# Kernel tuning notes

Measured on AMD Instinct MI355X. Metric: run time of the kernel, lower is better.

The kernel has to match this reference:

```python
import jax, jax.numpy as jnp
import numpy as np

DIM = 8
EPS = 1e-6
TRIL = DIM * (DIM + 1) // 2  # 36


def _build_L(params):
    # params: [N, TRIL] -> lower-triangular L: [N, DIM, DIM] with diag clamped >= 1e-4
    rows, cols = jnp.tril_indices(DIM)
    L = jnp.zeros((params.shape[0], DIM, DIM), params.dtype)
    L = L.at[:, rows, cols].set(params)
    idx = jnp.arange(DIM)
    d = jnp.clip(L[:, idx, idx], 0.0001)
    return L.at[:, idx, idx].set(d)


def _compute_density(L):
    # L: [N, DIM, DIM] -> PSD trace-1 density matrices [N, DIM, DIM]
    I = jnp.eye(DIM, dtype=L.dtype)
    rho = jnp.einsum('nij,nkj->nik', L, L) + EPS * I
    w = jnp.linalg.eigvalsh(rho)                      # [N, DIM]
    corr = jnp.maximum(-w.min(axis=-1), 0.0) + 1e-6   # shift to PSD
    rho = rho + corr[:, None, None] * I
    tr = jnp.trace(rho, axis1=1, axis2=2)
    return rho / (tr[:, None, None] + EPS)


def _matrix_sqrt(x):
    U, S, Vh = jnp.linalg.svd(x, full_matrices=False)
    sqrt_S = jnp.sqrt(S + EPS)
    return (U * sqrt_S[..., None, :]) @ Vh


def _quantum_fidelity(rho, sigma):
    sqrt_rho = _matrix_sqrt(rho)
    product = sqrt_rho @ sigma @ sqrt_rho
    S = jnp.linalg.svd(product, compute_uv=False)
    f = jnp.sum(jnp.sqrt(S + EPS), axis=-1)
    return jnp.clip(f, 0.0, 1.0)


def setup_inputs() -> dict:
    key = jax.random.key(0)
    k1, k2, k3 = jax.random.split(key, 3)
    B, S, V = 16384, 10, 100000
    contexts = jax.random.randint(k1, (B, S), 0, V)
    targets = jax.random.randint(k2, (B,), 0, V)
    # embedding table, init roughly like the torch module (uniform + diag ramp)
    emb_weight = jax.random.uniform(k3, (V, TRIL), jnp.float32, -0.1, 0.1)
    diag_idx = np.array([i * (i + 1) // 2 + i for i in range(DIM)])
    diag_vals = jnp.linspace(0.1, 1.0, DIM, dtype=jnp.float32)
    emb_weight = emb_weight.at[:, diag_idx].set(jnp.broadcast_to(diag_vals, (V, DIM)))
    return {"contexts": contexts, "targets": targets, "emb_weight": emb_weight}


def reference(contexts, targets, emb_weight):
    B, S = contexts.shape
    # context density matrices
    ctx_params = jnp.take(emb_weight, contexts.reshape(-1), axis=0)   # [B*S, TRIL]
    rho_ctx = _compute_density(_build_L(ctx_params)).reshape(B, S, DIM, DIM)
    mask = (contexts != 0).astype(rho_ctx.dtype)[:, :, None, None]
    context_rho = (rho_ctx * mask).sum(axis=1) / mask.sum(axis=1)     # [B, DIM, DIM]
    # target density matrices
    tgt_params = jnp.take(emb_weight, targets, axis=0)                # [B, TRIL]
    rho_tgt = _compute_density(_build_L(tgt_params))                  # [B, DIM, DIM]
    f = _quantum_fidelity(context_rho, rho_tgt)                       # [B]
    return -jnp.log(jnp.clip(f, 1e-8))
```

## Files before the change

kernel.cpp:

```cpp
#include <hip/hip_runtime.h>
#include <math.h>

#define NB   16384
#define SEQ  10
#define DIM  8
#define TRIL 36

__device__ __forceinline__ constexpr int tri(int r, int c) { return r * (r + 1) / 2 + c; }

__device__ __forceinline__ double fast_rsqrt(double x) {
    double r = __builtin_amdgcn_rsq(x);
    r = r * (1.5 - 0.5 * x * r * r);
    r = r * (1.5 - 0.5 * x * r * r);
    return r;
}
__device__ __forceinline__ double fast_rcp(double x) {
    double r = __builtin_amdgcn_rcp(x);
    r = r * (2.0 - x * r);
    r = r * (2.0 - x * r);
    return r;
}
__device__ __forceinline__ double fast_sqrt(double x) { return x * fast_rsqrt(x); }

template <bool ACCUM>
__device__ __forceinline__ void add_density(const float* __restrict__ p, double (&dst)[TRIL]) {
    double L[TRIL];
    #pragma unroll
    for (int i = 0; i < TRIL; ++i) L[i] = (double)p[i];
    #pragma unroll
    for (int d = 0; d < DIM; ++d) L[tri(d, d)] = fmax(L[tri(d, d)], 1.0e-4);

    double tr = 1.6e-5;
    #pragma unroll
    for (int i = 0; i < TRIL; ++i) tr += L[i] * L[i];
    double inv = fast_rcp(tr + 1.0e-6);

    #pragma unroll
    for (int i = 0; i < DIM; ++i) {
        #pragma unroll
        for (int j = 0; j <= i; ++j) {
            double sum = (i == j) ? 2.0e-6 : 0.0;
            #pragma unroll
            for (int k = 0; k <= j; ++k) sum += L[tri(i, k)] * L[tri(j, k)];
            if (ACCUM) dst[tri(i, j)] += sum * inv;
            else       dst[tri(i, j)]  = sum * inv;
        }
    }
}

__global__ void __launch_bounds__(64)
qcbow_kernel(const int* __restrict__ contexts,
             const int* __restrict__ targets,
             const float* __restrict__ emb,
             float* __restrict__ out)
{
    int b = blockIdx.x * 64 + threadIdx.x;

    double A[TRIL];
    #pragma unroll
    for (int i = 0; i < TRIL; ++i) A[i] = 0.0;
    double cnt = 0.0;

    for (int s = 0; s < SEQ; ++s) {
        int tok = contexts[b * SEQ + s];
        if (tok != 0) {
            add_density<true>(emb + (size_t)tok * TRIL, A);
            cnt += 1.0;
        }
    }
    double invc = fast_rcp(cnt);
    #pragma unroll
    for (int i = 0; i < TRIL; ++i) A[i] *= invc;
    #pragma unroll
    for (int d = 0; d < DIM; ++d) A[tri(d, d)] += 1.0e-6;

    double sig[TRIL];
    add_density<false>(emb + (size_t)targets[b] * TRIL, sig);

    #pragma unroll
    for (int j = 0; j < DIM; ++j) {
        double d = A[tri(j, j)];
        #pragma unroll
        for (int k = 0; k < j; ++k) d -= A[tri(j, k)] * A[tri(j, k)];
        d = fmax(d, 1.0e-30);
        double invd = fast_rsqrt(d);
        A[tri(j, j)] = d * invd;
        #pragma unroll
        for (int i = j + 1; i < DIM; ++i) {
            double v = A[tri(i, j)];
            #pragma unroll
            for (int k = 0; k < j; ++k) v -= A[tri(i, k)] * A[tri(j, k)];
            A[tri(i, j)] = v * invd;
        }
    }

    double C[TRIL];
    #pragma unroll
    for (int j = 0; j < DIM; ++j) {
        double w[DIM];
        #pragma unroll
        for (int k = 0; k < DIM; ++k) {
            double sum = 0.0;
            #pragma unroll
            for (int l = j; l < DIM; ++l) {
                double sk = (k >= l) ? sig[tri(k, l)] : sig[tri(l, k)];
                sum += sk * A[tri(l, j)];
            }
            w[k] = sum;
        }
        #pragma unroll
        for (int i = 0; i <= j; ++i) {
            double sum = 0.0;
            #pragma unroll
            for (int k = i; k < DIM; ++k) sum += A[tri(k, i)] * w[k];
            C[tri(j, i)] = sum;
        }
    }

    for (int sweep = 0; sweep < 8; ++sweep) {
        #pragma unroll
        for (int p = 0; p < DIM - 1; ++p) {
            #pragma unroll
            for (int q = p + 1; q < DIM; ++q) {
                double apq = C[tri(q, p)];
                if (fabs(apq) > 1.0e-20) {
                    double app = C[tri(p, p)];
                    double aqq = C[tri(q, q)];
                    float tauf = ((float)aqq - (float)app) * (0.5f * __builtin_amdgcn_rcpf((float)apq));
                    float tf = __builtin_amdgcn_rcpf(fabsf(tauf) + sqrtf(1.0f + tauf * tauf));
                    tf = (tauf >= 0.0f) ? tf : -tf;
                    double t = (double)tf;
                    double x = 1.0 + t * t;
                    double c = (double)__builtin_amdgcn_rsqf((float)x);
                    c = c * (1.5 - 0.5 * x * c * c);
                    double s = t * c;
                    double cc = c * c, ss = s * s, cs = c * s;
                    C[tri(p, p)] = cc * app + ss * aqq - 2.0 * cs * apq;
                    C[tri(q, q)] = ss * app + cc * aqq + 2.0 * cs * apq;
                    C[tri(q, p)] = cs * (app - aqq) + (cc - ss) * apq;
                    #pragma unroll
                    for (int k = 0; k < DIM; ++k) {
                        if (k == p || k == q) continue;
                        const int ikp = (k > p) ? tri(k, p) : tri(p, k);
                        const int ikq = (k > q) ? tri(k, q) : tri(q, k);
                        double akp = C[ikp];
                        double akq = C[ikq];
                        C[ikp] = c * akp - s * akq;
                        C[ikq] = s * akp + c * akq;
                    }
                }
            }
        }
        if (sweep >= 2) {
            double off2 = 0.0;
            #pragma unroll
            for (int i = 1; i < DIM; ++i) {
                #pragma unroll
                for (int j = 0; j < i; ++j) off2 += C[tri(i, j)] * C[tri(i, j)];
            }
            if (__all(off2 < 1.0e-14)) break;
        }
    }

    double f = 0.0;
    #pragma unroll
    for (int d = 0; d < DIM; ++d) f += fast_sqrt(fabs(C[tri(d, d)]) + 1.0e-6);
    f = fmin(f, 1.0);
    f = fmax(f, 1.0e-8);
    out[b] = (float)(-log(f));
}

extern "C" void kernel_launch(void* const* d_in, const int* in_sizes, int n_in,
                              void* d_out, int out_size, void* d_ws, size_t ws_size,
                              hipStream_t stream) {
    const int*   contexts = (const int*)d_in[0];
    const int*   targets  = (const int*)d_in[1];
    const float* emb      = (const float*)d_in[2];
    float*       out      = (float*)d_out;

    qcbow_kernel<<<dim3(NB / 64), dim3(64), 0, stream>>>(contexts, targets, emb, out);
}
```

Before: 99.73 us.

## Split each batch item across four lanes with parallel one-sided Jacobi SVD

Each batch element is now handled by a group of four lanes instead of one thread. The lanes split the context tokens, combine their density sums with xor shuffles, and each Cholesky-factor the target matrix redundantly. Fidelity comes from a one-sided (Hestenes) Jacobi on the columns of L_A^T L_W, two columns per lane, rotated among lanes in a round-robin order, in place of a two-sided Jacobi on a packed symmetric matrix. Embedding rows are now read with float4 vector loads and kept in float registers. This gives four times as many threads and less serial work per thread, at the cost of redundant Cholesky work, shuffle traffic, and float4 loads that assume 16-byte alignment of 36-float rows (144 bytes, so this holds).

```diff
diff --git a/kernel.cpp b/kernel.cpp
--- a/kernel.cpp
+++ b/kernel.cpp
@@ -24,15 +24,19 @@
 
 template <bool ACCUM>
 __device__ __forceinline__ void add_density(const float* __restrict__ p, double (&dst)[TRIL]) {
-    double L[TRIL];
-    #pragma unroll
-    for (int i = 0; i < TRIL; ++i) L[i] = (double)p[i];
-    #pragma unroll
-    for (int d = 0; d < DIM; ++d) L[tri(d, d)] = fmax(L[tri(d, d)], 1.0e-4);
+    float Lf[TRIL];
+    const float4* p4 = (const float4*)p;
+    #pragma unroll
+    for (int i = 0; i < 9; ++i) {
+        float4 v = p4[i];
+        Lf[4*i+0] = v.x; Lf[4*i+1] = v.y; Lf[4*i+2] = v.z; Lf[4*i+3] = v.w;
+    }
+    #pragma unroll
+    for (int d = 0; d < DIM; ++d) Lf[tri(d, d)] = fmaxf(Lf[tri(d, d)], 1.0e-4f);
 
     double tr = 1.6e-5;
     #pragma unroll
-    for (int i = 0; i < TRIL; ++i) tr += L[i] * L[i];
+    for (int i = 0; i < TRIL; ++i) { double v = (double)Lf[i]; tr += v * v; }
     double inv = fast_rcp(tr + 1.0e-6);
 
     #pragma unroll
@@ -41,9 +45,28 @@
         for (int j = 0; j <= i; ++j) {
             double sum = (i == j) ? 2.0e-6 : 0.0;
             #pragma unroll
-            for (int k = 0; k <= j; ++k) sum += L[tri(i, k)] * L[tri(j, k)];
+            for (int k = 0; k <= j; ++k) sum += (double)Lf[tri(i, k)] * (double)Lf[tri(j, k)];
             if (ACCUM) dst[tri(i, j)] += sum * inv;
             else       dst[tri(i, j)]  = sum * inv;
+        }
+    }
+}
+
+__device__ __forceinline__ void chol36(double (&M)[TRIL]) {
+    #pragma unroll
+    for (int j = 0; j < DIM; ++j) {
+        double d = M[tri(j, j)];
+        #pragma unroll
+        for (int k = 0; k < j; ++k) d -= M[tri(j, k)] * M[tri(j, k)];
+        d = fmax(d, 1.0e-30);
+        double invd = fast_rsqrt(d);
+        M[tri(j, j)] = d * invd;
+        #pragma unroll
+        for (int i = j + 1; i < DIM; ++i) {
+            double v = M[tri(i, j)];
+            #pragma unroll
+            for (int k = 0; k < j; ++k) v -= M[tri(i, k)] * M[tri(j, k)];
+            M[tri(i, j)] = v * invd;
         }
     }
 }
@@ -54,120 +77,123 @@
              const float* __restrict__ emb,
              float* __restrict__ out)
 {
-    int b = blockIdx.x * 64 + threadIdx.x;
+    const int tid = blockIdx.x * 64 + threadIdx.x;
+    const int b = tid >> 2;
+    const int g = threadIdx.x & 3;
 
     double A[TRIL];
     #pragma unroll
     for (int i = 0; i < TRIL; ++i) A[i] = 0.0;
     double cnt = 0.0;
-
-    for (int s = 0; s < SEQ; ++s) {
+    for (int s = g; s < SEQ; s += 4) {
         int tok = contexts[b * SEQ + s];
         if (tok != 0) {
             add_density<true>(emb + (size_t)tok * TRIL, A);
             cnt += 1.0;
         }
     }
+
+    double W[TRIL];
+    add_density<false>(emb + (size_t)targets[b] * TRIL, W);
+
+    #pragma unroll
+    for (int i = 0; i < TRIL; ++i) A[i] += __shfl_xor(A[i], 1, 4);
+    cnt += __shfl_xor(cnt, 1, 4);
+    #pragma unroll
+    for (int i = 0; i < TRIL; ++i) A[i] += __shfl_xor(A[i], 2, 4);
+    cnt += __shfl_xor(cnt, 2, 4);
+
+    chol36(W);
+
     double invc = fast_rcp(cnt);
     #pragma unroll
     for (int i = 0; i < TRIL; ++i) A[i] *= invc;
     #pragma unroll
     for (int d = 0; d < DIM; ++d) A[tri(d, d)] += 1.0e-6;
-
-    double sig[TRIL];
-    add_density<false>(emb + (size_t)targets[b] * TRIL, sig);
-
-    #pragma unroll
-    for (int j = 0; j < DIM; ++j) {
-        double d = A[tri(j, j)];
-        #pragma unroll
-        for (int k = 0; k < j; ++k) d -= A[tri(j, k)] * A[tri(j, k)];
-        d = fmax(d, 1.0e-30);
-        double invd = fast_rsqrt(d);
-        A[tri(j, j)] = d * invd;
-        #pragma unroll
-        for (int i = j + 1; i < DIM; ++i) {
-            double v = A[tri(i, j)];
-            #pragma unroll
-            for (int k = 0; k < j; ++k) v -= A[tri(i, k)] * A[tri(j, k)];
-            A[tri(i, j)] = v * invd;
-        }
-    }
-
-    double C[TRIL];
-    #pragma unroll
-    for (int j = 0; j < DIM; ++j) {
-        double w[DIM];
-        #pragma unroll
-        for (int k = 0; k < DIM; ++k) {
-            double sum = 0.0;
-            #pragma unroll
-            for (int l = j; l < DIM; ++l) {
-                double sk = (k >= l) ? sig[tri(k, l)] : sig[tri(l, k)];
-                sum += sk * A[tri(l, j)];
+    chol36(A);
+
+    double wa[DIM], wb[DIM];
+#define PICKW(JA, JB)                                                              \
+    {                                                                              \
+        _Pragma("unroll")                                                          \
+        for (int k = 0; k < DIM; ++k) wa[k] = (k >= (JA)) ? W[tri(k, (JA))] : 0.0; \
+        _Pragma("unroll")                                                          \
+        for (int k = 0; k < DIM; ++k) wb[k] = (k >= (JB)) ? W[tri(k, (JB))] : 0.0; \
+    }
+    switch (g) {
+        case 0: PICKW(0, 1); break;
+        case 1: PICKW(2, 3); break;
+        case 2: PICKW(4, 5); break;
+        default: PICKW(6, 7); break;
+    }
+#undef PICKW
+
+    double a[DIM], bc[DIM];
+    #pragma unroll
+    for (int i = 0; i < DIM; ++i) {
+        double sa = 0.0, sb = 0.0;
+        #pragma unroll
+        for (int k = i; k < DIM; ++k) {
+            double lk = A[tri(k, i)];
+            sa += lk * wa[k];
+            sb += lk * wb[k];
+        }
+        a[i] = sa; bc[i] = sb;
+    }
+
+    for (int sweep = 0; sweep < 10; ++sweep) {
+        double maxz2 = 0.0;
+        #pragma unroll
+        for (int r = 0; r < 7; ++r) {
+            double x = 0.0, y = 0.0, z = 0.0;
+            #pragma unroll
+            for (int k = 0; k < DIM; ++k) {
+                x += a[k] * a[k];
+                y += bc[k] * bc[k];
+                z += a[k] * bc[k];
             }
-            w[k] = sum;
-        }
-        #pragma unroll
-        for (int i = 0; i <= j; ++i) {
-            double sum = 0.0;
-            #pragma unroll
-            for (int k = i; k < DIM; ++k) sum += A[tri(k, i)] * w[k];
-            C[tri(j, i)] = sum;
-        }
-    }
-
-    for (int sweep = 0; sweep < 8; ++sweep) {
-        #pragma unroll
-        for (int p = 0; p < DIM - 1; ++p) {
-            #pragma unroll
-            for (int q = p + 1; q < DIM; ++q) {
-                double apq = C[tri(q, p)];
-                if (fabs(apq) > 1.0e-20) {
-                    double app = C[tri(p, p)];
-                    double aqq = C[tri(q, q)];
-                    float tauf = ((float)aqq - (float)app) * (0.5f * __builtin_amdgcn_rcpf((float)apq));
-                    float tf = __builtin_amdgcn_rcpf(fabsf(tauf) + sqrtf(1.0f + tauf * tauf));
-                    tf = (tauf >= 0.0f) ? tf : -tf;
-                    double t = (double)tf;
-                    double x = 1.0 + t * t;
-                    double c = (double)__builtin_amdgcn_rsqf((float)x);
-                    c = c * (1.5 - 0.5 * x * c * c);
-                    double s = t * c;
-                    double cc = c * c, ss = s * s, cs = c * s;
-                    C[tri(p, p)] = cc * app + ss * aqq - 2.0 * cs * apq;
-                    C[tri(q, q)] = ss * app + cc * aqq + 2.0 * cs * apq;
-                    C[tri(q, p)] = cs * (app - aqq) + (cc - ss) * apq;
-                    #pragma unroll
-                    for (int k = 0; k < DIM; ++k) {
-                        if (k == p || k == q) continue;
-                        const int ikp = (k > p) ? tri(k, p) : tri(p, k);
-                        const int ikq = (k > q) ? tri(k, q) : tri(q, k);
-                        double akp = C[ikp];
-                        double akq = C[ikq];
-                        C[ikp] = c * akp - s * akq;
-                        C[ikq] = s * akp + c * akq;
-                    }
+            double z2 = z * z;
+            maxz2 = fmax(maxz2, z2);
+            if (z2 > 1.0e-20) {
+                float tauf = (float)(y - x) * (0.5f * __builtin_amdgcn_rcpf((float)z));
+                float tf = __builtin_amdgcn_rcpf(fabsf(tauf) + sqrtf(1.0f + tauf * tauf));
+                tf = (tauf >= 0.0f) ? tf : -tf;
+                double t = (double)tf;
+                double x2 = 1.0 + t * t;
+                double c = (double)__builtin_amdgcn_rsqf((float)x2);
+                c = c * (1.5 - 0.5 * x2 * c * c);
+                double s = t * c;
+                #pragma unroll
+                for (int k = 0; k < DIM; ++k) {
+                    double na = c * a[k] - s * bc[k];
+                    double nb = s * a[k] + c * bc[k];
+                    a[k] = na; bc[k] = nb;
                 }
             }
-        }
-        if (sweep >= 2) {
-            double off2 = 0.0;
-            #pragma unroll
-            for (int i = 1; i < DIM; ++i) {
-                #pragma unroll
-                for (int j = 0; j < i; ++j) off2 += C[tri(i, j)] * C[tri(i, j)];
+            #pragma unroll
+            for (int k = 0; k < DIM; ++k) {
+                double olda = a[k];
+                double sa = (g == 0) ? bc[k] : a[k];
+                double ta = __shfl(sa, (g + 3) & 3, 4);
+                double tb = __shfl(bc[k], (g + 1) & 3, 4);
+                a[k]  = (g == 0) ? olda : ta;
+                bc[k] = (g == 3) ? olda : tb;
             }
-            if (__all(off2 < 1.0e-14)) break;
-        }
-    }
-
-    double f = 0.0;
-    #pragma unroll
-    for (int d = 0; d < DIM; ++d) f += fast_sqrt(fabs(C[tri(d, d)]) + 1.0e-6);
-    f = fmin(f, 1.0);
-    f = fmax(f, 1.0e-8);
-    out[b] = (float)(-log(f));
+        }
+        if (sweep >= 2 && __all(maxz2 < 1.0e-18)) break;
+    }
+
+    double x = 0.0, y = 0.0;
+    #pragma unroll
+    for (int k = 0; k < DIM; ++k) { x += a[k] * a[k]; y += bc[k] * bc[k]; }
+    double fp = fast_sqrt(x + 1.0e-6) + fast_sqrt(y + 1.0e-6);
+    fp += __shfl_xor(fp, 1, 4);
+    fp += __shfl_xor(fp, 2, 4);
+    if (g == 0) {
+        double f = fmin(fp, 1.0);
+        f = fmax(f, 1.0e-8);
+        out[b] = (float)(-log(f));
+    }
 }
 
 extern "C" void kernel_launch(void* const* d_in, const int* in_sizes, int n_in,
@@ -178,5 +204,5 @@
     const float* emb      = (const float*)d_in[2];
     float*       out      = (float*)d_out;
 
-    qcbow_kernel<<<dim3(NB / 64), dim3(64), 0, stream>>>(contexts, targets, emb, out);
-}
+    qcbow_kernel<<<dim3(NB * 4 / 64), dim3(64), 0, stream>>>(contexts, targets, emb, out);
+}
```

Measured after the change: 94.98 us. -4.8%, faster.
